# Optimization experiments

Measured on AMD Instinct MI355X. Metric: run time of the kernel, lower is better.

The kernel has to match this reference:

```python
import jax, jax.numpy as jnp
import numpy as np


def _base_index(H, W, dtype=jnp.float32):
    # Homogeneous pixel coordinates (x, y, 1) per pixel, shape [H, W, 3].
    x = jnp.arange(W, dtype=dtype)
    y = jnp.arange(H, dtype=dtype)
    xx, yy = jnp.meshgrid(x, y)  # [H, W]
    return jnp.stack([xx, yy, jnp.ones_like(xx)], axis=-1)


def _bilinear_resample(image, coords):
    # image: [B, H, W, C]; coords: [B, H, W, 2] in (x, y) order (tf resampler convention).
    # Out-of-bounds corners contribute zero (zero padding), matching tfa.image.resampler.
    B, H, W, C = image.shape
    x = coords[..., 0]
    y = coords[..., 1]
    x0 = jnp.floor(x)
    y0 = jnp.floor(y)
    wx1 = x - x0
    wy1 = y - y0
    wx0 = 1.0 - wx1
    wy0 = 1.0 - wy1
    x0i = x0.astype(jnp.int32)
    y0i = y0.astype(jnp.int32)
    x1i = x0i + 1
    y1i = y0i + 1

    def corner(yi, xi, w):
        valid = (xi >= 0) & (xi < W) & (yi >= 0) & (yi < H)
        xc = jnp.clip(xi, 0, W - 1)
        yc = jnp.clip(yi, 0, H - 1)
        # gather per batch: [B, H, W, C]
        g = jax.vmap(lambda im, yy, xx: im[yy, xx])(image, yc, xc)
        return g * (w * valid.astype(image.dtype))[..., None]

    return (corner(y0i, x0i, wy0 * wx0) + corner(y0i, x1i, wy0 * wx1)
            + corner(y1i, x0i, wy1 * wx0) + corner(y1i, x1i, wy1 * wx1))


def setup_inputs() -> dict:
    key = jax.random.key(0)
    k1, k2, k3 = jax.random.split(key, 3)
    B, H, W, C = 4, 512, 640, 16
    image_tensor = jax.random.normal(k1, (B, H, W, C), dtype=jnp.float32)
    # positive depths around 1
    depth_tensor = 0.5 + jax.random.uniform(k2, (B, H, W), dtype=jnp.float32)
    # near-identity projective transform so sampled coords land mostly in-bounds
    eye = jnp.eye(4, dtype=jnp.float32)[None].repeat(B, axis=0)
    project_tensor = eye + 0.001 * jax.random.normal(k3, (B, 4, 4), dtype=jnp.float32)
    return {"image_tensor": image_tensor, "depth_tensor": depth_tensor,
            "project_tensor": project_tensor}


def reference(image_tensor, depth_tensor, project_tensor):
    B, H, W, C = image_tensor.shape
    base = _base_index(H, W, image_tensor.dtype)  # [H, W, 3]
    R = project_tensor[:, :3, :3]                 # [B, 3, 3]
    t = project_tensor[:, :3, 3]                  # [B, 3]
    # tf.tensordot(R, base, [-1,-1]) -> [B,3,H,W]; transpose -> [B,H,W,3]
    rotate = jnp.einsum('bij,hwj->bhwi', R, base)
    sample = rotate * depth_tensor[..., None] + t[:, None, None, :]  # [B,H,W,3]
    coords = sample[..., :2] / sample[..., 2:3]                       # [B,H,W,2] (x,y)
    return _bilinear_resample(image_tensor, coords)
```

## Files before the change

kernel.cpp:

```cpp
#include <hip/hip_runtime.h>

constexpr int B  = 4;
constexpr int H  = 512;
constexpr int Wd = 640;
constexpr int NPIX_IMG = H * Wd;
constexpr int BLOCK = 256;
constexpr int PIXB  = BLOCK / 4;
constexpr int BPR   = Wd / PIXB;
constexpr int BLOCKS_PER_IMG = H * BPR;
constexpr int GRID  = B * BLOCKS_PER_IMG;
constexpr int KPF   = 1024;
static_assert(Wd % PIXB == 0, "block tiles a row exactly");
static_assert(GRID * BLOCK * 16 == B * NPIX_IMG * 64, "prefetch covers image exactly");

typedef float f32x4 __attribute__((ext_vector_type(4)));

__global__ __launch_bounds__(256) void depth_project_kernel(
    const float* __restrict__ image,
    const float* __restrict__ depth,
    const float* __restrict__ proj,
    float4* __restrict__ out)
{
    const int blk = blockIdx.x;
    const int tix = threadIdx.x;

    const int b   = blk / BLOCKS_PER_IMG;
    const int rem = blk % BLOCKS_PER_IMG;
    const int h   = rem / BPR;
    const int wb  = (rem % BPR) * PIXB;

    const int c4 = tix & 3;
    const int pl = tix >> 2;
    const int w  = wb + pl;
    const int pix = (b * H + h) * Wd + w;

    const float d = depth[pix];

    const f32x4* img_v = (const f32x4*)image;
    f32x4 pf = {0.0f, 0.0f, 0.0f, 0.0f};
    float pfd = 0.0f;
    const int pblk = blk + KPF;
    if (pblk < GRID) {
        pf = img_v[pblk * BLOCK + tix];
        if (tix < PIXB) pfd = depth[pblk * PIXB + tix];
    }

    const float* P = proj + b * 16;
    const float x = (float)w;
    const float y = (float)h;

    float sx = (P[0] * x + P[1] * y + P[2])  * d + P[3];
    float sy = (P[4] * x + P[5] * y + P[6])  * d + P[7];
    float sz = (P[8] * x + P[9] * y + P[10]) * d + P[11];
    float cx = sx / sz;
    float cy = sy / sz;

    float x0f = floorf(cx), y0f = floorf(cy);
    float wx1 = cx - x0f,   wy1 = cy - y0f;
    float wx0 = 1.0f - wx1, wy0 = 1.0f - wy1;
    int x0 = (int)x0f, y0 = (int)y0f;
    int x1 = x0 + 1,   y1 = y0 + 1;

    float vx0 = (x0 >= 0 && x0 < Wd) ? 1.0f : 0.0f;
    float vx1 = (x1 >= 0 && x1 < Wd) ? 1.0f : 0.0f;
    float vy0 = (y0 >= 0 && y0 < H)  ? 1.0f : 0.0f;
    float vy1 = (y1 >= 0 && y1 < H)  ? 1.0f : 0.0f;

    int x0c = min(max(x0, 0), Wd - 1);
    int x1c = min(max(x1, 0), Wd - 1);
    int y0c = min(max(y0, 0), H - 1);
    int y1c = min(max(y1, 0), H - 1);

    float w00 = wy0 * wx0 * vy0 * vx0;
    float w01 = wy0 * wx1 * vy0 * vx1;
    float w10 = wy1 * wx0 * vy1 * vx0;
    float w11 = wy1 * wx1 * vy1 * vx1;

    const float4* img4 = (const float4*)image;
    const int base_b = b * (NPIX_IMG * 4);
    float4 g00 = img4[base_b + (y0c * Wd + x0c) * 4 + c4];
    float4 g01 = img4[base_b + (y0c * Wd + x1c) * 4 + c4];
    float4 g10 = img4[base_b + (y1c * Wd + x0c) * 4 + c4];
    float4 g11 = img4[base_b + (y1c * Wd + x1c) * 4 + c4];

    f32x4 r;
    r.x = g00.x * w00 + g01.x * w01 + g10.x * w10 + g11.x * w11;
    r.y = g00.y * w00 + g01.y * w01 + g10.y * w10 + g11.y * w11;
    r.z = g00.z * w00 + g01.z * w01 + g10.z * w10 + g11.z * w11;
    r.w = g00.w * w00 + g01.w * w01 + g10.w * w10 + g11.w * w11;

    f32x4* out_v = (f32x4*)out;
    __builtin_nontemporal_store(r, out_v + pix * 4 + c4);

    asm volatile("" :: "v"(pf.x), "v"(pf.y), "v"(pf.z), "v"(pf.w), "v"(pfd));
}

extern "C" void kernel_launch(void* const* d_in, const int* in_sizes, int n_in,
                              void* d_out, int out_size, void* d_ws, size_t ws_size,
                              hipStream_t stream) {
    const float* image = (const float*)d_in[0];
    const float* depth = (const float*)d_in[1];
    const float* proj  = (const float*)d_in[2];
    float4* out = (float4*)d_out;

    depth_project_kernel<<<GRID, BLOCK, 0, stream>>>(image, depth, proj, out);
}
```

Before: 154.4 us.

## Replace in-kernel lookahead prefetch with separate cache-warming pre-pass kernel

Removes the per-block lookahead prefetch of image and depth data from the main gather kernel. Adds a separate streaming kernel, launched first, that reads the whole image and depth arrays so they sit in the large last-level cache before the gather kernel runs. The intent is to turn the irregular bilinear gathers into cache hits with fewer wasted loads inside the main kernel. The cost is an extra kernel launch and a full extra pass over the input data.

```diff
diff --git a/kernel.cpp b/kernel.cpp
--- a/kernel.cpp
+++ b/kernel.cpp
@@ -9,11 +9,39 @@
 constexpr int BPR   = Wd / PIXB;
 constexpr int BLOCKS_PER_IMG = H * BPR;
 constexpr int GRID  = B * BLOCKS_PER_IMG;
-constexpr int KPF   = 1024;
+
+constexpr int IMG_F4 = B * NPIX_IMG * 4;
+constexpr int DEP_F4 = B * NPIX_IMG / 4;
+constexpr int WARM_GRID = 2048;
+
 static_assert(Wd % PIXB == 0, "block tiles a row exactly");
-static_assert(GRID * BLOCK * 16 == B * NPIX_IMG * 64, "prefetch covers image exactly");
 
 typedef float f32x4 __attribute__((ext_vector_type(4)));
+
+
+__global__ __launch_bounds__(256) void warm_kernel(
+    const float* __restrict__ image,
+    const float* __restrict__ depth)
+{
+    const f32x4* img = (const f32x4*)image;
+    const f32x4* dep = (const f32x4*)depth;
+    const int stride = WARM_GRID * BLOCK;
+    int i = blockIdx.x * BLOCK + threadIdx.x;
+
+    f32x4 acc0 = {0.f, 0.f, 0.f, 0.f};
+    f32x4 acc1 = {0.f, 0.f, 0.f, 0.f};
+    for (; i + stride < IMG_F4; i += 2 * stride) {
+        f32x4 a = img[i];
+        f32x4 b2 = img[i + stride];
+        acc0 += a; acc1 += b2;
+    }
+    if (i < IMG_F4) acc0 += img[i];
+    for (int j = blockIdx.x * BLOCK + threadIdx.x; j < DEP_F4; j += stride)
+        acc1 += dep[j];
+
+    acc0 += acc1;
+    asm volatile("" :: "v"(acc0.x), "v"(acc0.y), "v"(acc0.z), "v"(acc0.w));
+}
 
 __global__ __launch_bounds__(256) void depth_project_kernel(
     const float* __restrict__ image,
@@ -35,15 +63,6 @@
     const int pix = (b * H + h) * Wd + w;
 
     const float d = depth[pix];
-
-    const f32x4* img_v = (const f32x4*)image;
-    f32x4 pf = {0.0f, 0.0f, 0.0f, 0.0f};
-    float pfd = 0.0f;
-    const int pblk = blk + KPF;
-    if (pblk < GRID) {
-        pf = img_v[pblk * BLOCK + tix];
-        if (tix < PIXB) pfd = depth[pblk * PIXB + tix];
-    }
 
     const float* P = proj + b * 16;
     const float x = (float)w;
@@ -91,8 +110,6 @@
 
     f32x4* out_v = (f32x4*)out;
     __builtin_nontemporal_store(r, out_v + pix * 4 + c4);
-
-    asm volatile("" :: "v"(pf.x), "v"(pf.y), "v"(pf.z), "v"(pf.w), "v"(pfd));
 }
 
 extern "C" void kernel_launch(void* const* d_in, const int* in_sizes, int n_in,
@@ -103,5 +120,6 @@
     const float* proj  = (const float*)d_in[2];
     float4* out = (float4*)d_out;
 
+    warm_kernel<<<WARM_GRID, BLOCK, 0, stream>>>(image, depth);
     depth_project_kernel<<<GRID, BLOCK, 0, stream>>>(image, depth, proj, out);
 }
```

Result: slower. 173.7 us (+12.5%).
